# Performance work log

Hardware: AMD Instinct MI355X
Metric: run time of the kernel (lower is better)

Reference implementation:

```python
import math
import jax, jax.numpy as jnp
import numpy as np

FACTOR = 2  # init kwarg `factor`

def setup_inputs() -> dict:
    key = jax.random.key(0)
    k1, k2, k3 = jax.random.split(key, 3)
    B, H, L, E = 32, 8, 2048, 64
    Q = jax.random.normal(k1, (B, H, L, E), dtype=jnp.float32)
    K = jax.random.normal(k2, (B, H, L, E), dtype=jnp.float32)
    V = jax.random.normal(k3, (B, H, L, E), dtype=jnp.float32)
    return {"Q": Q, "K": K, "V": V}

def _autocorrelation(Q, K, V):
    # Q, K, V: [B, H, L, E]; S == L so the pad/truncate branch is a no-op.
    B, H, L, E = Q.shape
    # FFT-based cross-correlation along the time axis (dim=2)
    q_fft = jnp.fft.rfft(Q, axis=2)
    k_fft = jnp.fft.rfft(K, axis=2)
    corr = jnp.fft.irfft(q_fft * jnp.conj(k_fft), n=L, axis=2)  # [B,H,L,E]
    # time_delay_agg
    top_k = int(FACTOR * math.log(L))  # = 15 for L=2048
    # torch.topk over dim=2 per (b,h,e): move L to last axis for lax.top_k
    weights, delays = jax.lax.top_k(jnp.swapaxes(corr, 2, 3), top_k)  # [B,H,E,k]
    weights = jax.nn.softmax(weights, axis=-1)
    # V.repeat(1,1,2,1) + gather(init+delay) is equivalent to a circular
    # gather from V with index (l + delay) mod L, since 0 <= init+delay <= 2L-2.
    base = jnp.arange(L)  # [L]
    out = jnp.zeros_like(V)
    for i in range(top_k):  # small fixed loop over top_k delays
        d_i = delays[..., i]                       # [B,H,E]
        idx = (base[None, None, :, None] + d_i[:, :, None, :]) % L  # [B,H,L,E]
        pattern = jnp.take_along_axis(V, idx, axis=2)               # [B,H,L,E]
        out = out + pattern * weights[..., i][:, :, None, :]
    return out

def reference(Q, K, V):
    return _autocorrelation(Q, K, V)
```

## Files before the change

### kernel.cpp

```cpp
#include <hip/hip_runtime.h>
#include <math.h>


#define LEN   2048
#define BH    256
#define NE    64
#define NSER  (BH * NE)
#define TOPK  15
#define NINF  (-INFINITY)

__device__ __forceinline__ int IDX(int i) { return i + (i >> 4); }

__device__ __forceinline__ void cmulf(float xr, float xi, float yr, float yi,
                                      float& zr, float& zi) {
  zr = xr * yr - xi * yi;
  zi = xr * yi + xi * yr;
}

__device__ __forceinline__ void sincos_tw(int idx, float& c, float& s) {
  float ang = (float)idx * (-6.283185307179586f / 2048.0f);
  __sincosf(ang, &s, &c);
}

template <bool INV>
__device__ __forceinline__ void dft8(float* xr, float* xi) {
  const float sg = INV ? -1.f : 1.f;
  const float c = 0.70710678118654752440f;
  float s0r = xr[0] + xr[4], s0i = xi[0] + xi[4];
  float s1r = xr[0] - xr[4], s1i = xi[0] - xi[4];
  float s2r = xr[2] + xr[6], s2i = xi[2] + xi[6];
  float s3r = xr[2] - xr[6], s3i = xi[2] - xi[6];
  float E0r = s0r + s2r, E0i = s0i + s2i;
  float E2r = s0r - s2r, E2i = s0i - s2i;
  float E1r = s1r + sg * s3i, E1i = s1i - sg * s3r;
  float E3r = s1r - sg * s3i, E3i = s1i + sg * s3r;
  float u0r = xr[1] + xr[5], u0i = xi[1] + xi[5];
  float u1r = xr[1] - xr[5], u1i = xi[1] - xi[5];
  float u2r = xr[3] + xr[7], u2i = xi[3] + xi[7];
  float u3r = xr[3] - xr[7], u3i = xi[3] - xi[7];
  float O0r = u0r + u2r, O0i = u0i + u2i;
  float O2r = u0r - u2r, O2i = u0i - u2i;
  float O1r = u1r + sg * u3i, O1i = u1i - sg * u3r;
  float O3r = u1r - sg * u3i, O3i = u1i + sg * u3r;
  float G0r = O0r, G0i = O0i;
  float G1r, G1i; cmulf(O1r, O1i, c, -sg * c, G1r, G1i);
  float G2r = sg * O2i, G2i = -sg * O2r;
  float G3r, G3i; cmulf(O3r, O3i, -c, -sg * c, G3r, G3i);
  xr[0] = E0r + G0r; xi[0] = E0i + G0i;
  xr[1] = E1r + G1r; xi[1] = E1i + G1i;
  xr[2] = E2r + G2r; xi[2] = E2i + G2i;
  xr[3] = E3r + G3r; xi[3] = E3i + G3i;
  xr[4] = E0r - G0r; xi[4] = E0i - G0i;
  xr[5] = E1r - G1r; xi[5] = E1i - G1i;
  xr[6] = E2r - G2r; xi[6] = E2i - G2i;
  xr[7] = E3r - G3r; xi[7] = E3i - G3i;
}

template <bool INV>
__device__ __forceinline__ void dft4(float* xr, float* xi) {
  const float sg = INV ? -1.f : 1.f;
  float s0r = xr[0] + xr[2], s0i = xi[0] + xi[2];
  float s1r = xr[0] - xr[2], s1i = xi[0] - xi[2];
  float s2r = xr[1] + xr[3], s2i = xi[1] + xi[3];
  float s3r = xr[1] - xr[3], s3i = xi[1] - xi[3];
  xr[0] = s0r + s2r;        xi[0] = s0i + s2i;
  xr[1] = s1r + sg * s3i;   xi[1] = s1i - sg * s3r;
  xr[2] = s0r - s2r;        xi[2] = s0i - s2i;
  xr[3] = s1r - sg * s3i;   xi[3] = s1i + sg * s3r;
}

template <bool INV>
__device__ __forceinline__ void stage8_ip(float* Re, float* Im,
                                          int s, int sLog, int t) {
  float ar[8], ai[8];
#pragma unroll
  for (int r = 0; r < 8; ++r) {
    int a = t + 256 * r;
    ar[r] = Re[IDX(a)]; ai[r] = Im[IDX(a)];
  }
  __syncthreads();
  dft8<INV>(ar, ai);
  int q = t & (s - 1), p = t >> sLog;
  int ob = q + 8 * s * p;
  int tb = s * p;
#pragma unroll
  for (int j = 0; j < 8; ++j) {
    float c_, s_;
    sincos_tw(tb * j, c_, s_);
    if (INV) s_ = -s_;
    float zr, zi; cmulf(ar[j], ai[j], c_, s_, zr, zi);
    int o = ob + s * j;
    Re[IDX(o)] = zr; Im[IDX(o)] = zi;
  }
  __syncthreads();
}


__global__ __launch_bounds__(256) void ktrans_qk(const float* __restrict__ Q,
                                                 const float* __restrict__ K,
                                                 float2* __restrict__ ZT) {
  int bh = blockIdx.x >> 5, l0 = (blockIdx.x & 31) * 64;
  __shared__ float sq[64][65], sk[64][65];
  int t = threadIdx.x;
  const float4* Qb = (const float4*)(Q + ((size_t)bh * LEN + l0) * NE);
  const float4* Kb = (const float4*)(K + ((size_t)bh * LEN + l0) * NE);
  int x = t & 15, c4 = x * 4;
#pragma unroll
  for (int it = 0; it < 4; ++it) {
    int row = (t >> 4) + it * 16;
    float4 q4 = Qb[row * 16 + x];
    float4 k4 = Kb[row * 16 + x];
    sq[row][c4 + 0] = q4.x; sq[row][c4 + 1] = q4.y;
    sq[row][c4 + 2] = q4.z; sq[row][c4 + 3] = q4.w;
    sk[row][c4 + 0] = k4.x; sk[row][c4 + 1] = k4.y;
    sk[row][c4 + 2] = k4.z; sk[row][c4 + 3] = k4.w;
  }
  __syncthreads();
  float2* Zb = ZT + (size_t)bh * NE * LEN + l0;
  int l2 = (t & 31) * 2;
#pragma unroll
  for (int it = 0; it < 8; ++it) {
    int e = (t >> 5) + it * 8;
    float4 o;
    o.x = sq[l2][e];     o.y = sk[l2][e];
    o.z = sq[l2 + 1][e]; o.w = sk[l2 + 1][e];
    *(float4*)&Zb[(size_t)e * LEN + l2] = o;
  }
}

__global__ __launch_bounds__(256) void ktrans_v(const float* __restrict__ src,
                                                float* __restrict__ dst) {
  int bh = blockIdx.x >> 5, l0 = (blockIdx.x & 31) * 64;
  __shared__ float sT[64][65];
  int t = threadIdx.x;
  const float4* Sb = (const float4*)(src + ((size_t)bh * LEN + l0) * NE);
  int x = t & 15, c4 = x * 4;
#pragma unroll
  for (int it = 0; it < 4; ++it) {
    int row = (t >> 4) + it * 16;
    float4 v4 = Sb[row * 16 + x];
    sT[row][c4 + 0] = v4.x; sT[row][c4 + 1] = v4.y;
    sT[row][c4 + 2] = v4.z; sT[row][c4 + 3] = v4.w;
  }
  __syncthreads();
  float* Db = dst + (size_t)bh * NE * LEN + l0;
  int l4 = x * 4;
#pragma unroll
  for (int it = 0; it < 4; ++it) {
    int e = (t >> 4) + it * 16;
    float4 o;
    o.x = sT[l4 + 0][e]; o.y = sT[l4 + 1][e];
    o.z = sT[l4 + 2][e]; o.w = sT[l4 + 3][e];
    *(float4*)&Db[(size_t)e * LEN + l4] = o;
  }
}

__global__ __launch_bounds__(256) void ktrans_o(const float* __restrict__ OT,
                                                float* __restrict__ out) {
  int bh = blockIdx.x >> 5, l0 = (blockIdx.x & 31) * 64;
  __shared__ float sT[64][65];
  int t = threadIdx.x;
  const float* Sb = OT + (size_t)bh * NE * LEN + l0;
  int x = t & 15, l4 = x * 4;
#pragma unroll
  for (int it = 0; it < 4; ++it) {
    int e = (t >> 4) + it * 16;
    float4 v4 = *(const float4*)&Sb[(size_t)e * LEN + l4];
    sT[e][l4 + 0] = v4.x; sT[e][l4 + 1] = v4.y;
    sT[e][l4 + 2] = v4.z; sT[e][l4 + 3] = v4.w;
  }
  __syncthreads();
  float* Ob = out + ((size_t)bh * LEN + l0) * NE;
  int e4 = x * 4;
#pragma unroll
  for (int it = 0; it < 4; ++it) {
    int row = (t >> 4) + it * 16;
    float4 o;
    o.x = sT[e4 + 0][row]; o.y = sT[e4 + 1][row];
    o.z = sT[e4 + 2][row]; o.w = sT[e4 + 3][row];
    *(float4*)&Ob[row * NE + e4] = o;
  }
}


__global__ __launch_bounds__(256, 8) void kfft(const float2* __restrict__ ZT,
                                               float* __restrict__ Wt,
                                               int* __restrict__ Dl) {
  __shared__ float Re[2176], Im[2176];
  __shared__ float mv[64]; __shared__ int mi[64];
  const int t = threadIdx.x;
  const int wv = t >> 6, ln = t & 63;
  const float2* z = ZT + (size_t)blockIdx.x * LEN;

  {
    float ar[8], ai[8];
#pragma unroll
    for (int r = 0; r < 8; ++r) {
      float2 v = z[t + 256 * r];
      ar[r] = v.x; ai[r] = v.y;
    }
    dft8<false>(ar, ai);
#pragma unroll
    for (int j = 0; j < 8; ++j) {
      float c_, s_;
      sincos_tw(t * j, c_, s_);
      float zr, zi; cmulf(ar[j], ai[j], c_, s_, zr, zi);
      int o = 8 * t + j;
      Re[IDX(o)] = zr; Im[IDX(o)] = zi;
    }
  }
  __syncthreads();
  stage8_ip<false>(Re, Im, 8, 3, t);
  stage8_ip<false>(Re, Im, 64, 6, t);
#pragma unroll
  for (int h = 0; h < 2; ++h) {
    int u = t + 256 * h;
    float xr[4], xi[4];
#pragma unroll
    for (int r = 0; r < 4; ++r) {
      int a = u + 512 * r;
      xr[r] = Re[IDX(a)]; xi[r] = Im[IDX(a)];
    }
    dft4<false>(xr, xi);
#pragma unroll
    for (int j = 0; j < 4; ++j) {
      int o = u + 512 * j;
      Re[IDX(o)] = xr[j]; Im[IDX(o)] = xi[j];
    }
  }
  __syncthreads();

  {
    float zfr[4], zfi[4], zmr[4], zmi[4];
#pragma unroll
    for (int r = 0; r < 4; ++r) {
      int f = t + 256 * r;
      int m = (LEN - f) & (LEN - 1);
      zfr[r] = Re[IDX(f)]; zfi[r] = Im[IDX(f)];
      zmr[r] = Re[IDX(m)]; zmi[r] = Im[IDX(m)];
    }
    float e1r = 0.f, e1i = 0.f;
    if (t == 0) { e1r = Re[IDX(1024)]; e1i = Im[IDX(1024)]; }
    __syncthreads();
#pragma unroll
    for (int r = 0; r < 4; ++r) {
      int f = t + 256 * r;
      int m = (LEN - f) & (LEN - 1);
      float Xr = 0.5f * (zfr[r] + zmr[r]), Xi = 0.5f * (zfi[r] - zmi[r]);
      float Yr = 0.5f * (zfi[r] + zmi[r]), Yi = -0.5f * (zfr[r] - zmr[r]);
      Re[IDX(f)] = Xr * Yr + Xi * Yi;
      Im[IDX(f)] = Xi * Yr - Xr * Yi;
      float Xr2 = 0.5f * (zmr[r] + zfr[r]), Xi2 = 0.5f * (zmi[r] - zfi[r]);
      float Yr2 = 0.5f * (zfi[r] + zmi[r]), Yi2 = -0.5f * (zmr[r] - zfr[r]);
      Re[IDX(m)] = Xr2 * Yr2 + Xi2 * Yi2;
      Im[IDX(m)] = Xi2 * Yr2 - Xr2 * Yi2;
    }
    if (t == 0) {
      Re[IDX(1024)] = e1r * e1i;
      Im[IDX(1024)] = 0.f;
    }
  }
  __syncthreads();

  stage8_ip<true>(Re, Im, 1, 0, t);
  stage8_ip<true>(Re, Im, 8, 3, t);
  stage8_ip<true>(Re, Im, 64, 6, t);
  float rv[8];
#pragma unroll
  for (int h = 0; h < 2; ++h) {
    int u = t + 256 * h;
    float xr[4], xi[4];
#pragma unroll
    for (int r = 0; r < 4; ++r) {
      int a = u + 512 * r;
      xr[r] = Re[IDX(a)]; xi[r] = Im[IDX(a)];
    }
    dft4<true>(xr, xi);
#pragma unroll
    for (int j = 0; j < 4; ++j) rv[h * 4 + j] = xr[j];
  }

  for (int it = 0; it < TOPK; ++it) {
    float bv = rv[0]; int bidx = t;
#pragma unroll
    for (int k = 1; k < 8; ++k) {
      int ik = t + 256 * (k >> 2) + 512 * (k & 3);
      bool btr = (rv[k] > bv) || (rv[k] == bv && ik < bidx);
      if (btr) { bv = rv[k]; bidx = ik; }
    }
#pragma unroll
    for (int off = 32; off >= 1; off >>= 1) {
      float ov = __shfl_xor(bv, off);
      int oi = __shfl_xor(bidx, off);
      bool btr = (ov > bv) || (ov == bv && oi < bidx);
      if (btr) { bv = ov; bidx = oi; }
    }
    if (ln == 0) { mv[wv * 16 + it] = bv; mi[wv * 16 + it] = bidx; }
    int d = bidx - t;
#pragma unroll
    for (int k = 0; k < 8; ++k) {
      int ck = 256 * (k >> 2) + 512 * (k & 3);
      if (d == ck) rv[k] = NINF;
    }
  }
  __syncthreads();

  if (wv == 0) {
    float v = ((ln & 15) < TOPK) ? mv[ln] : NINF;
    int ix = ((ln & 15) < TOPK) ? mi[ln] : 0;
    float myv = NINF; int myi = 0;
    for (int it = 0; it < TOPK; ++it) {
      float bv = v; int bidx = ix;
#pragma unroll
      for (int off = 32; off >= 1; off >>= 1) {
        float ov = __shfl_xor(bv, off);
        int oi = __shfl_xor(bidx, off);
        bool btr = (ov > bv) || (ov == bv && oi < bidx);
        if (btr) { bv = ov; bidx = oi; }
      }
      if (ln == it) { myv = bv; myi = bidx; }
      if (ix == bidx) v = NINF;
    }
    const float scl = 1.0f / 2048.0f;
    float vmax = __shfl(myv, 0);
    float e = (ln < TOPK) ? expf((myv - vmax) * scl) : 0.f;
    float ssum = e;
#pragma unroll
    for (int off = 1; off < 16; off <<= 1) ssum += __shfl_xor(ssum, off);
    if (ln < TOPK) {
      Wt[(size_t)blockIdx.x * 16 + ln] = e / ssum;
      Dl[(size_t)blockIdx.x * 16 + ln] = myi;
    }
  }
}


__global__ __launch_bounds__(256) void kgather(const float* __restrict__ VT,
                                               const float* __restrict__ Wt,
                                               const int* __restrict__ Dl,
                                               float* __restrict__ OT) {
  __shared__ float v[LEN];
  const int t = threadIdx.x;
  const int series = blockIdx.x;
  const float4* src = (const float4*)(VT + (size_t)series * LEN);
  float4* vv = (float4*)v;
#pragma unroll
  for (int i = 0; i < 2; ++i) vv[t + 256 * i] = src[t + 256 * i];
  float w[TOPK]; int d[TOPK];
#pragma unroll
  for (int i = 0; i < TOPK; ++i) {
    w[i] = Wt[(size_t)series * 16 + i];
    d[i] = Dl[(size_t)series * 16 + i];
  }
  __syncthreads();
  float* dst = OT + (size_t)series * LEN;
#pragma unroll
  for (int r = 0; r < 8; ++r) {
    int l = t + 256 * r;
    float acc = 0.f;
#pragma unroll
    for (int i = 0; i < TOPK; ++i) acc += w[i] * v[(l + d[i]) & (LEN - 1)];
    dst[l] = acc;
  }
}

extern "C" void kernel_launch(void* const* d_in, const int* in_sizes, int n_in,
                              void* d_out, int out_size, void* d_ws, size_t ws_size,
                              hipStream_t stream) {
  const float* Q = (const float*)d_in[0];
  const float* K = (const float*)d_in[1];
  const float* V = (const float*)d_in[2];
  float* out = (float*)d_out;
  char* ws = (char*)d_ws;

  const size_t ZT_BYTES = (size_t)NSER * LEN * sizeof(float2);
  float2* ZT = (float2*)ws;
  float* Wt = (float*)(ws + ZT_BYTES);
  int* Dl = (int*)(ws + ZT_BYTES + (size_t)NSER * 16 * sizeof(float));
  float* OT = (float*)ws;
  float* VT = out;

  ktrans_qk<<<BH * 32, 256, 0, stream>>>(Q, K, ZT);
  kfft<<<NSER, 256, 0, stream>>>(ZT, Wt, Dl);
  ktrans_v<<<BH * 32, 256, 0, stream>>>(V, VT);
  kgather<<<NSER, 256, 0, stream>>>(VT, Wt, Dl, OT);
  ktrans_o<<<BH * 32, 256, 0, stream>>>(OT, out);
}
```

Measured before the change: 885.7 us.

## Fuse output transpose into gather, interleave FFT smem, sort-based top-k

```diff
diff --git a/kernel.cpp b/kernel.cpp
--- a/kernel.cpp
+++ b/kernel.cpp
@@ -9,13 +9,7 @@
 #define TOPK  15
 #define NINF  (-INFINITY)
 
-__device__ __forceinline__ int IDX(int i) { return i + (i >> 4); }
-
-__device__ __forceinline__ void cmulf(float xr, float xi, float yr, float yi,
-                                      float& zr, float& zi) {
-  zr = xr * yr - xi * yi;
-  zi = xr * yi + xi * yr;
-}
+__device__ __forceinline__ int PC(int c) { return c + (c >> 4); }
 
 __device__ __forceinline__ void sincos_tw(int idx, float& c, float& s) {
   float ang = (float)idx * (-6.283185307179586f / 2048.0f);
@@ -43,9 +37,9 @@
   float O1r = u1r + sg * u3i, O1i = u1i - sg * u3r;
   float O3r = u1r - sg * u3i, O3i = u1i + sg * u3r;
   float G0r = O0r, G0i = O0i;
-  float G1r, G1i; cmulf(O1r, O1i, c, -sg * c, G1r, G1i);
+  float G1r = O1r * c + O1i * (sg * c), G1i = O1i * c - O1r * (sg * c);
   float G2r = sg * O2i, G2i = -sg * O2r;
-  float G3r, G3i; cmulf(O3r, O3i, -c, -sg * c, G3r, G3i);
+  float G3r = -O3r * c + O3i * (sg * c), G3i = -O3i * c - O3r * (sg * c);
   xr[0] = E0r + G0r; xi[0] = E0i + G0i;
   xr[1] = E1r + G1r; xi[1] = E1i + G1i;
   xr[2] = E2r + G2r; xi[2] = E2i + G2i;
@@ -70,27 +64,31 @@
 }
 
 template <bool INV>
-__device__ __forceinline__ void stage8_ip(float* Re, float* Im,
-                                          int s, int sLog, int t) {
+__device__ __forceinline__ void stage8_ip(float2* CB, int s, int sLog, int t) {
   float ar[8], ai[8];
 #pragma unroll
   for (int r = 0; r < 8; ++r) {
-    int a = t + 256 * r;
-    ar[r] = Re[IDX(a)]; ai[r] = Im[IDX(a)];
+    float2 v = CB[PC(t + 256 * r)];
+    ar[r] = v.x; ai[r] = v.y;
   }
   __syncthreads();
   dft8<INV>(ar, ai);
   int q = t & (s - 1), p = t >> sLog;
   int ob = q + 8 * s * p;
-  int tb = s * p;
-#pragma unroll
-  for (int j = 0; j < 8; ++j) {
-    float c_, s_;
-    sincos_tw(tb * j, c_, s_);
-    if (INV) s_ = -s_;
-    float zr, zi; cmulf(ar[j], ai[j], c_, s_, zr, zi);
-    int o = ob + s * j;
-    Re[IDX(o)] = zr; Im[IDX(o)] = zi;
+  float c1, s1; sincos_tw(s * p, c1, s1);
+  if (INV) s1 = -s1;
+  CB[PC(ob)] = make_float2(ar[0], ai[0]);
+  float wc = c1, wsn = s1;
+#pragma unroll
+  for (int j = 1; j < 8; ++j) {
+    float zr = ar[j] * wc - ai[j] * wsn;
+    float zi = ar[j] * wsn + ai[j] * wc;
+    CB[PC(ob + s * j)] = make_float2(zr, zi);
+    if (j < 7) {
+      float nc = wc * c1 - wsn * s1;
+      wsn = wc * s1 + wsn * c1;
+      wc = nc;
+    }
   }
   __syncthreads();
 }
@@ -155,38 +153,11 @@
   }
 }
 
-__global__ __launch_bounds__(256) void ktrans_o(const float* __restrict__ OT,
-                                                float* __restrict__ out) {
-  int bh = blockIdx.x >> 5, l0 = (blockIdx.x & 31) * 64;
-  __shared__ float sT[64][65];
-  int t = threadIdx.x;
-  const float* Sb = OT + (size_t)bh * NE * LEN + l0;
-  int x = t & 15, l4 = x * 4;
-#pragma unroll
-  for (int it = 0; it < 4; ++it) {
-    int e = (t >> 4) + it * 16;
-    float4 v4 = *(const float4*)&Sb[(size_t)e * LEN + l4];
-    sT[e][l4 + 0] = v4.x; sT[e][l4 + 1] = v4.y;
-    sT[e][l4 + 2] = v4.z; sT[e][l4 + 3] = v4.w;
-  }
-  __syncthreads();
-  float* Ob = out + ((size_t)bh * LEN + l0) * NE;
-  int e4 = x * 4;
-#pragma unroll
-  for (int it = 0; it < 4; ++it) {
-    int row = (t >> 4) + it * 16;
-    float4 o;
-    o.x = sT[e4 + 0][row]; o.y = sT[e4 + 1][row];
-    o.z = sT[e4 + 2][row]; o.w = sT[e4 + 3][row];
-    *(float4*)&Ob[row * NE + e4] = o;
-  }
-}
-
-
-__global__ __launch_bounds__(256, 8) void kfft(const float2* __restrict__ ZT,
+
+__global__ __launch_bounds__(256, 6) void kfft(const float2* __restrict__ ZT,
                                                float* __restrict__ Wt,
                                                int* __restrict__ Dl) {
-  __shared__ float Re[2176], Im[2176];
+  __shared__ float2 CB[2176];
   __shared__ float mv[64]; __shared__ int mi[64];
   const int t = threadIdx.x;
   const int wv = t >> 6, ln = t & 63;
@@ -200,94 +171,99 @@
       ar[r] = v.x; ai[r] = v.y;
     }
     dft8<false>(ar, ai);
-#pragma unroll
-    for (int j = 0; j < 8; ++j) {
-      float c_, s_;
-      sincos_tw(t * j, c_, s_);
-      float zr, zi; cmulf(ar[j], ai[j], c_, s_, zr, zi);
-      int o = 8 * t + j;
-      Re[IDX(o)] = zr; Im[IDX(o)] = zi;
-    }
-  }
-  __syncthreads();
-  stage8_ip<false>(Re, Im, 8, 3, t);
-  stage8_ip<false>(Re, Im, 64, 6, t);
+    float c1, s1; sincos_tw(t, c1, s1);
+    CB[PC(8 * t)] = make_float2(ar[0], ai[0]);
+    float wc = c1, wsn = s1;
+#pragma unroll
+    for (int j = 1; j < 8; ++j) {
+      float zr = ar[j] * wc - ai[j] * wsn;
+      float zi = ar[j] * wsn + ai[j] * wc;
+      CB[PC(8 * t + j)] = make_float2(zr, zi);
+      if (j < 7) {
+        float nc = wc * c1 - wsn * s1;
+        wsn = wc * s1 + wsn * c1;
+        wc = nc;
+      }
+    }
+  }
+  __syncthreads();
+  stage8_ip<false>(CB, 8, 3, t);
+  stage8_ip<false>(CB, 64, 6, t);
 #pragma unroll
   for (int h = 0; h < 2; ++h) {
     int u = t + 256 * h;
     float xr[4], xi[4];
 #pragma unroll
     for (int r = 0; r < 4; ++r) {
-      int a = u + 512 * r;
-      xr[r] = Re[IDX(a)]; xi[r] = Im[IDX(a)];
+      float2 v = CB[PC(u + 512 * r)];
+      xr[r] = v.x; xi[r] = v.y;
     }
     dft4<false>(xr, xi);
 #pragma unroll
-    for (int j = 0; j < 4; ++j) {
-      int o = u + 512 * j;
-      Re[IDX(o)] = xr[j]; Im[IDX(o)] = xi[j];
-    }
+    for (int j = 0; j < 4; ++j) CB[PC(u + 512 * j)] = make_float2(xr[j], xi[j]);
   }
   __syncthreads();
 
   {
-    float zfr[4], zfi[4], zmr[4], zmi[4];
+    float2 zf[4], zm[4];
 #pragma unroll
     for (int r = 0; r < 4; ++r) {
       int f = t + 256 * r;
       int m = (LEN - f) & (LEN - 1);
-      zfr[r] = Re[IDX(f)]; zfi[r] = Im[IDX(f)];
-      zmr[r] = Re[IDX(m)]; zmi[r] = Im[IDX(m)];
-    }
-    float e1r = 0.f, e1i = 0.f;
-    if (t == 0) { e1r = Re[IDX(1024)]; e1i = Im[IDX(1024)]; }
+      zf[r] = CB[PC(f)]; zm[r] = CB[PC(m)];
+    }
+    float2 e1 = make_float2(0.f, 0.f);
+    if (t == 0) e1 = CB[PC(1024)];
     __syncthreads();
 #pragma unroll
     for (int r = 0; r < 4; ++r) {
       int f = t + 256 * r;
       int m = (LEN - f) & (LEN - 1);
-      float Xr = 0.5f * (zfr[r] + zmr[r]), Xi = 0.5f * (zfi[r] - zmi[r]);
-      float Yr = 0.5f * (zfi[r] + zmi[r]), Yi = -0.5f * (zfr[r] - zmr[r]);
-      Re[IDX(f)] = Xr * Yr + Xi * Yi;
-      Im[IDX(f)] = Xi * Yr - Xr * Yi;
-      float Xr2 = 0.5f * (zmr[r] + zfr[r]), Xi2 = 0.5f * (zmi[r] - zfi[r]);
-      float Yr2 = 0.5f * (zfi[r] + zmi[r]), Yi2 = -0.5f * (zmr[r] - zfr[r]);
-      Re[IDX(m)] = Xr2 * Yr2 + Xi2 * Yi2;
-      Im[IDX(m)] = Xi2 * Yr2 - Xr2 * Yi2;
-    }
-    if (t == 0) {
-      Re[IDX(1024)] = e1r * e1i;
-      Im[IDX(1024)] = 0.f;
-    }
-  }
-  __syncthreads();
-
-  stage8_ip<true>(Re, Im, 1, 0, t);
-  stage8_ip<true>(Re, Im, 8, 3, t);
-  stage8_ip<true>(Re, Im, 64, 6, t);
-  float rv[8];
+      float Xr = 0.5f * (zf[r].x + zm[r].x), Xi = 0.5f * (zf[r].y - zm[r].y);
+      float Yr = 0.5f * (zf[r].y + zm[r].y), Yi = -0.5f * (zf[r].x - zm[r].x);
+      CB[PC(f)] = make_float2(Xr * Yr + Xi * Yi, Xi * Yr - Xr * Yi);
+      float Xr2 = 0.5f * (zm[r].x + zf[r].x), Xi2 = 0.5f * (zm[r].y - zf[r].y);
+      float Yr2 = 0.5f * (zf[r].y + zm[r].y), Yi2 = -0.5f * (zm[r].x - zf[r].x);
+      CB[PC(m)] = make_float2(Xr2 * Yr2 + Xi2 * Yi2, Xi2 * Yr2 - Xr2 * Yi2);
+    }
+    if (t == 0) CB[PC(1024)] = make_float2(e1.x * e1.y, 0.f);
+  }
+  __syncthreads();
+
+  stage8_ip<true>(CB, 1, 0, t);
+  stage8_ip<true>(CB, 8, 3, t);
+  stage8_ip<true>(CB, 64, 6, t);
+  float rv[8]; int ri[8];
 #pragma unroll
   for (int h = 0; h < 2; ++h) {
     int u = t + 256 * h;
     float xr[4], xi[4];
 #pragma unroll
     for (int r = 0; r < 4; ++r) {
-      int a = u + 512 * r;
-      xr[r] = Re[IDX(a)]; xi[r] = Im[IDX(a)];
+      float2 v = CB[PC(u + 512 * r)];
+      xr[r] = v.x; xi[r] = v.y;
     }
     dft4<true>(xr, xi);
 #pragma unroll
-    for (int j = 0; j < 4; ++j) rv[h * 4 + j] = xr[j];
-  }
+    for (int j = 0; j < 4; ++j) {
+      rv[h * 4 + j] = xr[j];
+      ri[h * 4 + j] = u + 512 * j;
+    }
+  }
+
+#define CE(i, j) { bool sw = rv[i] < rv[j];                                   \
+    float tv = sw ? rv[j] : rv[i]; rv[j] = sw ? rv[i] : rv[j]; rv[i] = tv;    \
+    int tx = sw ? ri[j] : ri[i];  ri[j] = sw ? ri[i] : ri[j];  ri[i] = tx; }
+  CE(0,1) CE(2,3) CE(4,5) CE(6,7)
+  CE(0,2) CE(1,3) CE(4,6) CE(5,7)
+  CE(1,2) CE(5,6)
+  CE(0,4) CE(1,5) CE(2,6) CE(3,7)
+  CE(2,4) CE(3,5)
+  CE(1,2) CE(3,4) CE(5,6)
+#undef CE
 
   for (int it = 0; it < TOPK; ++it) {
-    float bv = rv[0]; int bidx = t;
-#pragma unroll
-    for (int k = 1; k < 8; ++k) {
-      int ik = t + 256 * (k >> 2) + 512 * (k & 3);
-      bool btr = (rv[k] > bv) || (rv[k] == bv && ik < bidx);
-      if (btr) { bv = rv[k]; bidx = ik; }
-    }
+    float bv = rv[0]; int bidx = ri[0];
 #pragma unroll
     for (int off = 32; off >= 1; off >>= 1) {
       float ov = __shfl_xor(bv, off);
@@ -296,11 +272,10 @@
       if (btr) { bv = ov; bidx = oi; }
     }
     if (ln == 0) { mv[wv * 16 + it] = bv; mi[wv * 16 + it] = bidx; }
-    int d = bidx - t;
-#pragma unroll
-    for (int k = 0; k < 8; ++k) {
-      int ck = 256 * (k >> 2) + 512 * (k & 3);
-      if (d == ck) rv[k] = NINF;
+    if (bidx == ri[0]) {
+#pragma unroll
+      for (int k = 0; k < 7; ++k) { rv[k] = rv[k + 1]; ri[k] = ri[k + 1]; }
+      rv[7] = NINF;
     }
   }
   __syncthreads();
@@ -335,32 +310,34 @@
 }
 
 
-__global__ __launch_bounds__(256) void kgather(const float* __restrict__ VT,
-                                               const float* __restrict__ Wt,
-                                               const int* __restrict__ Dl,
-                                               float* __restrict__ OT) {
+__global__ __launch_bounds__(256) void kgather_out(const float* __restrict__ VT,
+                                                   const float* __restrict__ Wt,
+                                                   const int* __restrict__ Dl,
+                                                   float* __restrict__ out) {
+  const int w = blockIdx.x;
+  const int s = (w & 7) * 2048 + (w >> 3);
+  const int bh = s >> 6, e = s & 63;
   __shared__ float v[LEN];
   const int t = threadIdx.x;
-  const int series = blockIdx.x;
-  const float4* src = (const float4*)(VT + (size_t)series * LEN);
+  const float4* src = (const float4*)(VT + (size_t)s * LEN);
   float4* vv = (float4*)v;
 #pragma unroll
   for (int i = 0; i < 2; ++i) vv[t + 256 * i] = src[t + 256 * i];
-  float w[TOPK]; int d[TOPK];
+  float wgt[TOPK]; int d[TOPK];
 #pragma unroll
   for (int i = 0; i < TOPK; ++i) {
-    w[i] = Wt[(size_t)series * 16 + i];
-    d[i] = Dl[(size_t)series * 16 + i];
-  }
-  __syncthreads();
-  float* dst = OT + (size_t)series * LEN;
+    wgt[i] = Wt[(size_t)s * 16 + i];
+    d[i] = Dl[(size_t)s * 16 + i];
+  }
+  __syncthreads();
+  float* dst = out + ((size_t)bh * LEN) * NE + e;
 #pragma unroll
   for (int r = 0; r < 8; ++r) {
     int l = t + 256 * r;
     float acc = 0.f;
 #pragma unroll
-    for (int i = 0; i < TOPK; ++i) acc += w[i] * v[(l + d[i]) & (LEN - 1)];
-    dst[l] = acc;
+    for (int i = 0; i < TOPK; ++i) acc += wgt[i] * v[(l + d[i]) & (LEN - 1)];
+    dst[(size_t)l * NE] = acc;
   }
 }
 
@@ -377,12 +354,10 @@
   float2* ZT = (float2*)ws;
   float* Wt = (float*)(ws + ZT_BYTES);
   int* Dl = (int*)(ws + ZT_BYTES + (size_t)NSER * 16 * sizeof(float));
-  float* OT = (float*)ws;
-  float* VT = out;
+  float* VT = (float*)ws;
 
   ktrans_qk<<<BH * 32, 256, 0, stream>>>(Q, K, ZT);
   kfft<<<NSER, 256, 0, stream>>>(ZT, Wt, Dl);
   ktrans_v<<<BH * 32, 256, 0, stream>>>(V, VT);
-  kgather<<<NSER, 256, 0, stream>>>(VT, Wt, Dl, OT);
-  ktrans_o<<<BH * 32, 256, 0, stream>>>(OT, out);
-}
+  kgather_out<<<NSER, 256, 0, stream>>>(VT, Wt, Dl, out);
+}
```

Result: faster. 859.0 us (-3.0%).
